# Performance work log

Hardware: AMD Instinct MI355X
Metric: run time of the kernel (lower is better)

## Reference

```python
import jax, jax.numpy as jnp
import numpy as np

SIGNAL_DIM = 64   # D
STATE_DIM = 64    # N
SEQ_LEN = 16384   # L
BATCH = 16


def _init_dplr_hippo(state_dim):
    """NumPy port of init_DPLR_HiPPO(signal_dim=1, state_dim). Returns Lambda,(N,) P,(N,) B,(N,1) complex64."""
    n = np.arange(state_dim, dtype=np.float64)
    A = np.zeros((state_dim, state_dim))
    for k in range(state_dim):
        A[k:, k] = np.sqrt(2.0 * np.arange(k, state_dim) + 1.0) * np.sqrt(2.0 * k + 1.0)
        A[k, k] = k + 1
    A = -A
    P = np.sqrt(n + 0.5)
    SI = A + P[:, None] * P[None, :]
    diag = np.diagonal(SI).copy()
    S = SI - np.diag(diag)
    eigvals, V = np.linalg.eigh(S * -1j)   # S*-1j is Hermitian
    Lam = diag + 1j * eigvals
    Vc = V.conj().T
    Pc = Vc @ P.astype(np.complex128)
    B = np.sqrt(2.0 * n + 1.0)[:, None]    # (N, 1): signal_dim=1, tied across channels
    Bc = Vc @ B.astype(np.complex128)
    return Lam.astype(np.complex64), Pc.astype(np.complex64), Bc.astype(np.complex64)


def _ri(x):
    # complex -> (..., 2) float32, matching torch.view_as_real parameter storage
    return jnp.stack([jnp.real(x), jnp.imag(x)], axis=-1).astype(jnp.float32)


def _to_c(x):
    return jax.lax.complex(x[..., 0], x[..., 1])


def setup_inputs() -> dict:
    key = jax.random.key(0)
    ku, kc1, kc2, kd, ks = jax.random.split(key, 5)
    Lam, P, B = _init_dplr_hippo(STATE_DIM)
    C = (jax.random.normal(kc1, (SIGNAL_DIM, STATE_DIM)) +
         1j * jax.random.normal(kc2, (SIGNAL_DIM, STATE_DIM))).astype(jnp.complex64)
    return {
        "u": jax.random.normal(ku, (BATCH, SEQ_LEN, SIGNAL_DIM), dtype=jnp.float32),
        "Lambda_ri": _ri(jnp.asarray(Lam)),      # (N, 2)
        "P_ri": _ri(jnp.asarray(P)),             # (N, 2)
        "B_ri": _ri(jnp.asarray(B)),             # (N, 1, 2)
        "C_ri": _ri(C),                          # (D, N, 2)
        "D_param": jax.random.normal(kd, (SIGNAL_DIM,), dtype=jnp.float32),
        "log_step": jnp.log(jax.random.uniform(ks, (1,), minval=0.001, maxval=0.1)).astype(jnp.float32),
    }


def reference(u, Lambda_ri, P_ri, B_ri, C_ri, D_param, log_step):
    Lam = _to_c(Lambda_ri)   # (N,)
    P = _to_c(P_ri)          # (N,)
    B = _to_c(B_ri)          # (N, 1)
    C = _to_c(C_ri)          # (D, N)
    L = u.shape[-2]

    step = jnp.exp(log_step)                                  # (1,)
    Omega = jnp.exp(-2j * jnp.pi * (jnp.arange(L) / L))       # (L,) roots of unity
    g = (2.0 / step) * ((1.0 - Omega) / (1.0 + Omega))        # (L,)

    # Batched Cauchy kernel: k_ab[l] = sum_n a_n * b_n / (g_l - Lambda_n)
    cauchy = 1.0 / (g[:, None] - Lam[None, :])                # (L, N)
    a0 = jnp.conj(C)        # (D, N)
    a1 = jnp.conj(P)        # (N,)
    b0 = B[:, 0]            # (N,)  == B.T row (signal_dim=1)
    b1 = P                  # (N,)
    k00 = jnp.einsum('dn,n,ln->dl', a0, b0, cauchy)
    k01 = jnp.einsum('dn,n,ln->dl', a0, b1, cauchy)
    k10 = jnp.einsum('n,n,ln->l', a1, b0, cauchy)
    k11 = jnp.einsum('n,n,ln->l', a1, b1, cauchy)

    evaluated = (2.0 / (1.0 + Omega)) * (k00 - k01 * (1.0 / (1.0 + k11)) * k10)  # (D, L)
    K = jnp.fft.ifft(evaluated, axis=-1).T.real               # (L, D) conv kernel

    # FFT convolution along time axis (zero-pad to 2L, linear convolution)
    ud = jnp.fft.rfft(jnp.pad(u, ((0, 0), (0, L), (0, 0))), axis=-2)
    Kd = jnp.fft.rfft(jnp.pad(K, ((0, L), (0, 0))), axis=-2)
    y = jnp.fft.irfft(ud * Kd, n=2 * L, axis=-2)[..., :L, :]
    return y + D_param * u
```

## Files before the change

kernel.cpp:

```cpp
#include <hip/hip_runtime.h>
#include <math.h>

#define MF 16384
#define HALF 8192

__device__ __forceinline__ float2 cmul(float2 a, float2 b){ return make_float2(a.x*b.x - a.y*b.y, a.x*b.y + a.y*b.x); }
__device__ __forceinline__ float2 cmulc(float2 a, float2 b){ return make_float2(a.x*b.x + a.y*b.y, a.y*b.x - a.x*b.y); }
__device__ __forceinline__ int rho4(int v){ return ((v & 3) << 2) | (v >> 2); }
__device__ __forceinline__ int sob(int k){
    return (rho4(k & 15) << 10) | (rho4((k >> 4) & 15) << 6) | (rho4((k >> 8) & 15) << 2) | (k >> 12);
}
__device__ __forceinline__ int ph(int e){ return e ^ ((e >> 4) & 3) ^ (((e >> 6) & 3) << 2); }

__device__ __forceinline__ void bf4f(float2&a,float2&b,float2&c,float2&d){
    float t0x=a.x+c.x, t0y=a.y+c.y, t2x=a.x-c.x, t2y=a.y-c.y;
    float t1x=b.x+d.x, t1y=b.y+d.y, t3x=b.x-d.x, t3y=b.y-d.y;
    a=make_float2(t0x+t1x,t0y+t1y);
    b=make_float2(t2x+t3y,t2y-t3x);
    c=make_float2(t0x-t1x,t0y-t1y);
    d=make_float2(t2x-t3y,t2y+t3x);
}
__device__ __forceinline__ void bf4i(float2&a,float2&b,float2&c,float2&d){
    float t0x=a.x+c.x, t0y=a.y+c.y, t2x=a.x-c.x, t2y=a.y-c.y;
    float t1x=b.x+d.x, t1y=b.y+d.y, t3x=b.x-d.x, t3y=b.y-d.y;
    a=make_float2(t0x+t1x,t0y+t1y);
    b=make_float2(t2x-t3y,t2y+t3x);
    c=make_float2(t0x-t1x,t0y-t1y);
    d=make_float2(t2x+t3y,t2y-t3x);
}

#define W16_1 make_float2(0.92387953251128674f, -0.38268343236508978f)
#define W16_2 make_float2(0.70710678118654752f, -0.70710678118654752f)
#define W16_3 make_float2(0.38268343236508978f, -0.92387953251128674f)
#define W16_6 make_float2(-0.70710678118654752f, -0.70710678118654752f)
#define W16_9 make_float2(-0.92387953251128674f, 0.38268343236508978f)

__device__ __forceinline__ void dft16_fwd(float2* x){
    bf4f(x[0],x[4],x[8],x[12]);
    bf4f(x[1],x[5],x[9],x[13]);
    bf4f(x[2],x[6],x[10],x[14]);
    bf4f(x[3],x[7],x[11],x[15]);
    x[5]=cmul(x[5],W16_1);  x[9]=cmul(x[9],W16_2);   x[13]=cmul(x[13],W16_3);
    x[6]=cmul(x[6],W16_2);  { float2 t=x[10]; x[10]=make_float2(t.y,-t.x); } x[14]=cmul(x[14],W16_6);
    x[7]=cmul(x[7],W16_3);  x[11]=cmul(x[11],W16_6); x[15]=cmul(x[15],W16_9);
    bf4f(x[0],x[1],x[2],x[3]);
    bf4f(x[4],x[5],x[6],x[7]);
    bf4f(x[8],x[9],x[10],x[11]);
    bf4f(x[12],x[13],x[14],x[15]);
}
__device__ __forceinline__ void dft16_inv(float2* x){
    bf4i(x[0],x[1],x[2],x[3]);
    bf4i(x[4],x[5],x[6],x[7]);
    bf4i(x[8],x[9],x[10],x[11]);
    bf4i(x[12],x[13],x[14],x[15]);
    x[5]=cmulc(x[5],W16_1); x[9]=cmulc(x[9],W16_2);  x[13]=cmulc(x[13],W16_3);
    x[6]=cmulc(x[6],W16_2); { float2 t=x[10]; x[10]=make_float2(-t.y,t.x); } x[14]=cmulc(x[14],W16_6);
    x[7]=cmulc(x[7],W16_3); x[11]=cmulc(x[11],W16_6); x[15]=cmulc(x[15],W16_9);
    bf4i(x[0],x[4],x[8],x[12]);
    bf4i(x[1],x[5],x[9],x[13]);
    bf4i(x[2],x[6],x[10],x[14]);
    bf4i(x[3],x[7],x[11],x[15]);
}

template<bool INV>
__device__ __forceinline__ void tw0_apply(float2* x, float2 w1){
    float2 w2=cmul(w1,w1), w4=cmul(w2,w2), w8=cmul(w4,w4);
    float2 w3=cmul(w2,w1), w5=cmul(w4,w1), w6=cmul(w4,w2), w7=cmul(w4,w3);
    float2 w9=cmul(w8,w1), w10=cmul(w8,w2), w11=cmul(w8,w3), w12=cmul(w8,w4);
    float2 w13=cmul(w8,w5), w14=cmul(w8,w6), w15=cmul(w8,w7);
    if (!INV){
        x[1]=cmul(x[1],w4);   x[2]=cmul(x[2],w8);   x[3]=cmul(x[3],w12);
        x[4]=cmul(x[4],w1);   x[5]=cmul(x[5],w5);   x[6]=cmul(x[6],w9);
        x[7]=cmul(x[7],w13);  x[8]=cmul(x[8],w2);   x[9]=cmul(x[9],w6);
        x[10]=cmul(x[10],w10);x[11]=cmul(x[11],w14);x[12]=cmul(x[12],w3);
        x[13]=cmul(x[13],w7); x[14]=cmul(x[14],w11);x[15]=cmul(x[15],w15);
    } else {
        x[1]=cmulc(x[1],w4);   x[2]=cmulc(x[2],w8);   x[3]=cmulc(x[3],w12);
        x[4]=cmulc(x[4],w1);   x[5]=cmulc(x[5],w5);   x[6]=cmulc(x[6],w9);
        x[7]=cmulc(x[7],w13);  x[8]=cmulc(x[8],w2);   x[9]=cmulc(x[9],w6);
        x[10]=cmulc(x[10],w10);x[11]=cmulc(x[11],w14);x[12]=cmulc(x[12],w3);
        x[13]=cmulc(x[13],w7); x[14]=cmulc(x[14],w11);x[15]=cmulc(x[15],w15);
    }
}

template<bool INV>
__device__ __forceinline__ void pass0(float2* A, float2 w1g, int tid){
    float2 x[16];
    int base = ph(tid);
    #pragma unroll
    for(int m=0;m<16;++m) x[m] = A[base + (m<<10)];
    if(!INV){ dft16_fwd(x); tw0_apply<false>(x, w1g); }
    else { tw0_apply<true>(x, w1g); dft16_inv(x); }
    #pragma unroll
    for(int m=0;m<16;++m) A[base + (m<<10)] = x[m];
}

template<bool INV>
__device__ __forceinline__ void pass1(float2* A, const float2* tw1s, int tid){
    float2 x[16];
    int i1 = tid & 63;
    int B = (tid >> 6) << 10;
    int i1x = i1 ^ ((i1 >> 4) & 3);
    int b0 = B | i1x;
    int b1 = B | 64 | (i1x ^ 4);
    int b2 = B | 128 | (i1x ^ 8);
    int b3 = B | 192 | (i1x ^ 12);
    x[0]=A[b0];     x[1]=A[b1];     x[2]=A[b2];     x[3]=A[b3];
    x[4]=A[b0+256]; x[5]=A[b1+256]; x[6]=A[b2+256]; x[7]=A[b3+256];
    x[8]=A[b0+512]; x[9]=A[b1+512]; x[10]=A[b2+512];x[11]=A[b3+512];
    x[12]=A[b0+768];x[13]=A[b1+768];x[14]=A[b2+768];x[15]=A[b3+768];
    if(!INV){
        dft16_fwd(x);
        #pragma unroll
        for(int j=1;j<16;++j) x[j] = cmul(x[j], tw1s[(j<<6)+i1]);
    } else {
        #pragma unroll
        for(int j=1;j<16;++j) x[j] = cmulc(x[j], tw1s[(j<<6)+i1]);
        dft16_inv(x);
    }
    A[b0]=x[0];     A[b1]=x[1];     A[b2]=x[2];     A[b3]=x[3];
    A[b0+256]=x[4]; A[b1+256]=x[5]; A[b2+256]=x[6]; A[b3+256]=x[7];
    A[b0+512]=x[8]; A[b1+512]=x[9]; A[b2+512]=x[10];A[b3+512]=x[11];
    A[b0+768]=x[12];A[b1+768]=x[13];A[b2+768]=x[14];A[b3+768]=x[15];
}

template<bool INV>
__device__ __forceinline__ void pass2(float2* A, const float2* tw2s, int tid){
    float2 x[16];
    int q = tid >> 2, j2 = tid & 3;
    int qb = q << 6, qa = q & 3;
    int c0 = qb | (j2 ^ 0);
    int c1 = qb | 16 | (j2 ^ 1);
    int c2 = qb | 32 | (j2 ^ 2);
    int c3 = qb | 48 | (j2 ^ 3);
    int r0 = (qa ^ 0) << 2, r1 = (qa ^ 1) << 2, r2 = (qa ^ 2) << 2, r3 = (qa ^ 3) << 2;
    x[0]=A[c0+r0];  x[1]=A[c0+r1];  x[2]=A[c0+r2];  x[3]=A[c0+r3];
    x[4]=A[c1+r0];  x[5]=A[c1+r1];  x[6]=A[c1+r2];  x[7]=A[c1+r3];
    x[8]=A[c2+r0];  x[9]=A[c2+r1];  x[10]=A[c2+r2]; x[11]=A[c2+r3];
    x[12]=A[c3+r0]; x[13]=A[c3+r1]; x[14]=A[c3+r2]; x[15]=A[c3+r3];
    if(!INV){
        dft16_fwd(x);
        #pragma unroll
        for(int j=1;j<16;++j) x[j] = cmul(x[j], tw2s[(j<<2)+j2]);
    } else {
        #pragma unroll
        for(int j=1;j<16;++j) x[j] = cmulc(x[j], tw2s[(j<<2)+j2]);
        dft16_inv(x);
    }
    A[c0+r0]=x[0];  A[c0+r1]=x[1];  A[c0+r2]=x[2];  A[c0+r3]=x[3];
    A[c1+r0]=x[4];  A[c1+r1]=x[5];  A[c1+r2]=x[6];  A[c1+r3]=x[7];
    A[c2+r0]=x[8];  A[c2+r1]=x[9];  A[c2+r2]=x[10]; A[c2+r3]=x[11];
    A[c3+r0]=x[12]; A[c3+r1]=x[13]; A[c3+r2]=x[14]; A[c3+r3]=x[15];
}

template<bool INV>
__device__ __forceinline__ void pass3(float2* A, int tid){
    int sgm = ((tid>>2)&3) ^ (((tid>>4)&3)<<2);
    #pragma unroll
    for(int rr=0; rr<4; ++rr){
        int base = (tid<<2) | (rr<<12);
        float2 a=A[(base|0)^sgm], b=A[(base|1)^sgm], c=A[(base|2)^sgm], d=A[(base|3)^sgm];
        if(!INV) bf4f(a,b,c,d); else bf4i(a,b,c,d);
        A[(base|0)^sgm]=a; A[(base|1)^sgm]=b; A[(base|2)^sgm]=c; A[(base|3)^sgm]=d;
    }
}

__global__ __launch_bounds__(1024) void k_evalinit(const float2* __restrict__ Lam, const float2* __restrict__ P,
        const float2* __restrict__ Bc, const float2* __restrict__ C,
        const float* __restrict__ log_step, float2* __restrict__ E,
        float2* __restrict__ baseg, float2* __restrict__ tw1g, float2* __restrict__ tw2g) {
    __shared__ float2 bTs[16][64];
    __shared__ float2 pTs[16][64];
    __shared__ float2 S10s[16], S11s[16];
    __shared__ float2 C_l[64][65];
    __shared__ float2 tile[16][65];
    int tid = threadIdx.x;
    if (blockIdx.x >= 256){
        const double TP = 6.2831853071795864769;
        double a = -TP * (double)tid / 16384.0;
        baseg[tid] = make_float2((float)cos(a), (float)sin(a));
        double a1 = -TP * (double)((tid & 63) * rho4(tid >> 6)) / 1024.0;
        tw1g[tid] = make_float2((float)cos(a1), (float)sin(a1));
        if (tid < 64){
            double a2 = -TP * (double)((tid & 3) * rho4(tid >> 2)) / 64.0;
            tw2g[tid] = make_float2((float)cos(a2), (float)sin(a2));
        }
        return;
    }
    int l0 = blockIdx.x * 64;
    float step = expf(log_step[0]);
    {
        int dq = tid >> 6, n = tid & 63;
        #pragma unroll
        for (int p = 0; p < 4; ++p) { int dd = dq + p * 16; C_l[n][dd] = C[dd * 64 + n]; }
    }
    __syncthreads();
    int w = tid >> 6;
    int lane = tid & 63;
    for (int p = 0; p < 4; ++p) {
        int l = l0 + p * 16 + w;
        float lf = (float)l * (1.0f / 16384.0f);
        float s2 = sinpif(lf), c2 = cospif(lf);
        float2 q1 = make_float2(2.0f*c2*c2, -2.0f*s2*c2);
        {
            int n = lane;
            float2 q2 = make_float2(4.0f*s2*s2, 4.0f*s2*c2);
            float2 ln = Lam[n];
            float2 lq = cmul(ln, q1);
            float2 den = make_float2(q2.x - step*lq.x, q2.y - step*lq.y);
            float idn = step / (den.x*den.x + den.y*den.y);
            float2 T = make_float2(den.x*idn, -den.y*idn);
            float2 bn = Bc[n], pn = P[n];
            float2 bT = cmul(bn, T), pT = cmul(pn, T);
            bTs[w][n] = bT; pTs[w][n] = pT;
            float2 s10 = make_float2(pn.x*bT.x + pn.y*bT.y, pn.x*bT.y - pn.y*bT.x);
            float2 s11 = make_float2(pn.x*pT.x + pn.y*pT.y, pn.x*pT.y - pn.y*pT.x);
            #pragma unroll
            for (int off = 32; off > 0; off >>= 1) {
                s10.x += __shfl_xor(s10.x, off);
                s10.y += __shfl_xor(s10.y, off);
                s11.x += __shfl_xor(s11.x, off);
                s11.y += __shfl_xor(s11.y, off);
            }
            if (n == 0) { S10s[w] = s10; S11s[w] = s11; }
        }
        __syncthreads();
        {
            int d = lane;
            float2 S00 = make_float2(0.f, 0.f), S01 = make_float2(0.f, 0.f);
            #pragma unroll 8
            for (int n = 0; n < 64; ++n) {
                float2 cn = C_l[n][d];
                float2 bT = bTs[w][n];
                float2 pT = pTs[w][n];
                S00.x += cn.x*bT.x + cn.y*bT.y;  S00.y += cn.x*bT.y - cn.y*bT.x;
                S01.x += cn.x*pT.x + cn.y*pT.y;  S01.y += cn.x*pT.y - cn.y*pT.x;
            }
            float2 S10 = S10s[w], S11 = S11s[w];
            float2 k11 = cmul(q1, S11); k11.x += 1.0f;
            float2 k10q = cmul(q1, S10);
            float ik = 1.0f / (k11.x*k11.x + k11.y*k11.y);
            float2 quo = make_float2((k10q.x*k11.x + k10q.y*k11.y) * ik,
                                     (k10q.y*k11.x - k10q.x*k11.y) * ik);
            float2 corr = cmul(S01, quo);
            tile[w][d] = make_float2(2.0f*(S00.x - corr.x), 2.0f*(S00.y - corr.y));
        }
        __syncthreads();
        {
            int lo = tid & 15, dq = tid >> 4;
            E[(size_t)dq * MF + l0 + p * 16 + lo] = tile[lo][dq];
        }
        __syncthreads();
    }
}

union MidShm {
    struct { float2 A[MF]; float2 tw1s[1024]; float2 tw2s[64]; } p;
    float t[256][65];
};

__global__ __launch_bounds__(1024) void k_mid(const float2* __restrict__ E, float4* __restrict__ Ktab,
        const float2* __restrict__ baseg, const float2* __restrict__ tw1g, const float2* __restrict__ tw2g,
        const float* __restrict__ u, float* __restrict__ uT) {
    __shared__ MidShm sh;
    int tid = threadIdx.x;
    if (blockIdx.x >= 64){
        int cid = blockIdx.x - 64;
        int b = cid >> 6, t0c = (cid & 63) << 8;
        const float* ub = u + ((size_t)(b * MF + t0c)) * 64;
        #pragma unroll
        for (int it = 0; it < 16; ++it){
            int tl = it * 16 + (tid >> 6), dl = tid & 63;
            sh.t[tl][dl] = ub[(size_t)tl * 64 + dl];
        }
        __syncthreads();
        float* dst = uT + (size_t)b * 64 * MF + t0c;
        #pragma unroll
        for (int it = 0; it < 16; ++it){
            int dd = (tid >> 8) + it * 4, tl = tid & 255;
            dst[(size_t)dd * MF + tl] = sh.t[tl][dd];
        }
        return;
    }
    float2* A = sh.p.A;
    float2* tw1s = sh.p.tw1s;
    float2* tw2s = sh.p.tw2s;
    float2 w1g = baseg[tid];
    tw1s[tid] = tw1g[tid];
    if (tid < 64) tw2s[tid] = tw2g[tid];
    int d = blockIdx.x;
    const float2* Ed = E + (size_t)d * MF;
    #pragma unroll
    for (int r = 0; r < 16; ++r) { int l = tid + (r << 10); A[ph(sob(l))] = Ed[l]; }
    __syncthreads();
    pass3<true>(A, tid); __syncthreads();
    pass2<true>(A, tw2s, tid); __syncthreads();
    pass1<true>(A, tw1s, tid); __syncthreads();
    pass0<true>(A, w1g, tid); __syncthreads();
    const float s = 1.0f / (float)MF;
    float2 rv[8];
    #pragma unroll
    for (int r = 0; r < 8; ++r) {
        int t = tid + (r << 10);
        rv[r] = make_float2(A[ph(2*t)].x * s, A[ph(2*t+1)].x * s);
    }
    __syncthreads();
    int pht = ph(tid);
    #pragma unroll
    for (int r = 0; r < 16; ++r) A[pht + (r << 10)] = (r < 8) ? rv[r] : make_float2(0.f, 0.f);
    __syncthreads();
    pass0<false>(A, w1g, tid); __syncthreads();
    pass1<false>(A, tw1s, tid); __syncthreads();
    pass2<false>(A, tw2s, tid); __syncthreads();
    pass3<false>(A, tid); __syncthreads();
    float4* Kd = Ktab + (size_t)d * MF;
    int Cbits = (rho4(tid >> 6) << 4) | (rho4((tid >> 2) & 15) << 8) | ((tid & 3) << 12);
    const float ksc = 1.0f / (float)MF;
    #pragma unroll
    for (int r = 0; r < 16; ++r) {
        int k = Cbits | rho4(r);
        int kp = (MF - k) & (MF - 1);
        int p = sob(kp);
        float kf = (float)k * (1.0f / 16384.0f);
        float2 w = make_float2(cospif(kf), -sinpif(kf));
        float2 Zk = A[pht + (r << 10)];
        float2 Zm = A[ph(p)]; Zm.y = -Zm.y;
        float2 Ue = make_float2(0.5f*(Zk.x + Zm.x), 0.5f*(Zk.y + Zm.y));
        float2 dd = make_float2(Zk.x - Zm.x, Zk.y - Zm.y);
        float2 Uo = make_float2(0.5f*dd.y, -0.5f*dd.x);
        float2 t2 = cmul(w, Uo);
        Kd[tid + (r << 10)] = make_float4((Ue.x + t2.x)*ksc, (Ue.y + t2.y)*ksc,
                                          (Ue.x - t2.x)*ksc, (Ue.y - t2.y)*ksc);
    }
}

template<bool TRANS>
__global__ __launch_bounds__(1024) void k_conv(const float* __restrict__ u, const float* __restrict__ uT,
        const float4* __restrict__ Ktab, const float* __restrict__ Dp,
        float* __restrict__ yT, float* __restrict__ yout,
        const float2* __restrict__ baseg, const float2* __restrict__ tw1g, const float2* __restrict__ tw2g) {
    __shared__ float2 A[MF];
    __shared__ float2 tw1s[1024];
    __shared__ float2 tw2s[64];
    int tid = threadIdx.x;
    float2 w1g = baseg[tid];
    tw1s[tid] = tw1g[tid];
    if (tid < 64) tw2s[tid] = tw2g[tid];
    int bid = blockIdx.x;
    int vb = ((bid & 7) << 7) | (bid >> 3);
    int d = vb >> 4, b = vb & 15;
    int bd = (b << 6) | d;
    int base = ph(tid);
    const float2* src = (const float2*)(uT + (size_t)bd * MF);
    const float* ub = u + ((size_t)b * MF) * 64 + d;
    {
        float2 x[16];
        #pragma unroll
        for (int m = 0; m < 16; ++m){
            if (m < 8){
                if (TRANS) x[m] = src[tid + (m << 10)];
                else { int t = tid + (m << 10); x[m] = make_float2(ub[(size_t)(2*t)*64], ub[(size_t)(2*t+1)*64]); }
            } else x[m] = make_float2(0.f, 0.f);
        }
        dft16_fwd(x);
        tw0_apply<false>(x, w1g);
        #pragma unroll
        for (int m = 0; m < 16; ++m) A[base + (m << 10)] = x[m];
    }
    __syncthreads();
    pass1<false>(A, tw1s, tid); __syncthreads();
    pass2<false>(A, tw2s, tid); __syncthreads();
    const float4* Kd = Ktab + (size_t)d * MF;
    float4 kd[16];
    #pragma unroll
    for (int r = 0; r < 16; ++r) kd[r] = Kd[tid + (r << 10)];
    pass3<false>(A, tid); __syncthreads();
    int Cbits = (rho4(tid >> 6) << 4) | (rho4((tid >> 2) & 15) << 8) | ((tid & 3) << 12);
    float2 Wr[16];
    #pragma unroll
    for (int r = 0; r < 16; ++r) {
        int k = Cbits | rho4(r);
        int kp = (MF - k) & (MF - 1);
        int p = sob(kp);
        float kf = (float)k * (1.0f / 16384.0f);
        float2 w = make_float2(cospif(kf), -sinpif(kf));
        float2 Zk = A[base + (r << 10)];
        float2 Zm = A[ph(p)]; Zm.y = -Zm.y;
        float2 Ue = make_float2(0.5f*(Zk.x + Zm.x), 0.5f*(Zk.y + Zm.y));
        float2 dd = make_float2(Zk.x - Zm.x, Zk.y - Zm.y);
        float2 Uo = make_float2(0.5f*dd.y, -0.5f*dd.x);
        float2 t2 = cmul(w, Uo);
        float2 X0 = make_float2(Ue.x + t2.x, Ue.y + t2.y);
        float2 X1 = make_float2(Ue.x - t2.x, Ue.y - t2.y);
        float2 Y0 = cmul(X0, make_float2(kd[r].x, kd[r].y));
        float2 Y1 = cmul(X1, make_float2(kd[r].z, kd[r].w));
        float2 Ey = make_float2(0.5f*(Y0.x + Y1.x), 0.5f*(Y0.y + Y1.y));
        float2 Dy = make_float2(Y0.x - Y1.x, Y0.y - Y1.y);
        float2 Oy = cmulc(Dy, w);
        Oy.x *= 0.5f; Oy.y *= 0.5f;
        Wr[r] = make_float2(Ey.x - Oy.y, Ey.y + Oy.x);
    }
    __syncthreads();
    #pragma unroll
    for (int r = 0; r < 16; ++r) A[base + (r << 10)] = Wr[r];
    __syncthreads();
    pass3<true>(A, tid); __syncthreads();
    pass2<true>(A, tw2s, tid); __syncthreads();
    pass1<true>(A, tw1s, tid); __syncthreads();
    {
        float2 x[16];
        #pragma unroll
        for (int m = 0; m < 16; ++m) x[m] = A[base + (m << 10)];
        tw0_apply<true>(x, w1g);
        dft16_inv(x);
        float Dd = Dp[d];
        if (TRANS){
            float2* dst = (float2*)(yT + (size_t)bd * MF);
            #pragma unroll
            for (int m = 0; m < 8; ++m){
                float2 s2 = src[tid + (m << 10)];
                dst[tid + (m << 10)] = make_float2(x[m].x + Dd * s2.x, x[m].y + Dd * s2.y);
            }
        } else {
            float* yb = yout + ((size_t)b * MF) * 64 + d;
            #pragma unroll
            for (int m = 0; m < 8; ++m){
                int t = tid + (m << 10);
                yb[(size_t)(2*t)*64]   = x[m].x + Dd * ub[(size_t)(2*t)*64];
                yb[(size_t)(2*t+1)*64] = x[m].y + Dd * ub[(size_t)(2*t+1)*64];
            }
        }
    }
}

__global__ void k_out(const float* __restrict__ yT, float* __restrict__ y) {
    __shared__ float tile[64][65];
    int b = blockIdx.y, t0 = blockIdx.x * 64, tid = threadIdx.x;
    #pragma unroll
    for (int k2 = 0; k2 < 16; ++k2) {
        int idx = tid + k2 * 256;
        int dl = idx >> 6, tl = idx & 63;
        tile[dl][tl] = yT[((size_t)b * 64 + dl) * MF + t0 + tl];
    }
    __syncthreads();
    #pragma unroll
    for (int k2 = 0; k2 < 16; ++k2) {
        int idx = tid + k2 * 256;
        int tl = idx >> 6, dl = idx & 63;
        y[((size_t)(b * MF + t0 + tl)) * 64 + dl] = tile[dl][tl];
    }
}

extern "C" void kernel_launch(void* const* d_in, const int* in_sizes, int n_in,
                              void* d_out, int out_size, void* d_ws, size_t ws_size,
                              hipStream_t stream) {
    const float*  u   = (const float*)d_in[0];
    const float2* Lam = (const float2*)d_in[1];
    const float2* P   = (const float2*)d_in[2];
    const float2* Bc  = (const float2*)d_in[3];
    const float2* C   = (const float2*)d_in[4];
    const float*  Dp  = (const float*)d_in[5];
    const float*  ls  = (const float*)d_in[6];
    float* y = (float*)d_out;
    char* ws = (char*)d_ws;

    size_t off = 0;
    float2* baseg = (float2*)(ws + off); off += (size_t)1024 * sizeof(float2);
    float2* tw1g  = (float2*)(ws + off); off += (size_t)1024 * sizeof(float2);
    float2* tw2g  = (float2*)(ws + off); off += (size_t)64 * sizeof(float2) + 512;
    float2* E     = (float2*)(ws + off); off += (size_t)64 * MF * sizeof(float2);
    float4* Ktab  = (float4*)(ws + off); off += (size_t)64 * MF * sizeof(float4);
    float*  uT    = (float*) (ws + off); off += (size_t)1024 * MF * sizeof(float);
    float*  yT    = (float*) (ws + off); off += (size_t)1024 * MF * sizeof(float);
    bool trans = (ws_size >= off);

    k_evalinit<<<257, 1024, 0, stream>>>(Lam, P, Bc, C, ls, E, baseg, tw1g, tw2g);
    k_mid<<<trans ? 1088 : 64, 1024, 0, stream>>>(E, Ktab, baseg, tw1g, tw2g, u, uT);

    if (trans) {
        k_conv<true><<<1024, 1024, 0, stream>>>(u, uT, Ktab, Dp, yT, y, baseg, tw1g, tw2g);
        k_out<<<dim3(MF / 64, 16), 256, 0, stream>>>(yT, y);
    } else {
        k_conv<false><<<1024, 1024, 0, stream>>>(u, nullptr, Ktab, Dp, nullptr, y, baseg, tw1g, tw2g);
    }
}
```

Before: 299.8 us.

## Fuse last FFT pass into pointwise multiply and compute twiddles by recurrence

In the convolution kernel, the final radix-4 forward pass and the first inverse pass are folded into the pointwise spectrum-multiply stage. This removes two shared-memory round trips and their barriers. Pass1 and pass2 twiddles are now derived from a single base twiddle per thread, which shrinks the shared twiddle tables, while k_mid keeps the old table-driven passes. The D*u skip term moves from k_conv into the k_out transpose kernel, which now reads u again from global memory in exchange for skipping the uT read in k_conv.

```diff
diff --git a/kernel.cpp b/kernel.cpp
--- a/kernel.cpp
+++ b/kernel.cpp
@@ -96,7 +96,7 @@
 }
 
 template<bool INV>
-__device__ __forceinline__ void pass1(float2* A, const float2* tw1s, int tid){
+__device__ __forceinline__ void pass1(float2* A, const float2* basP1, int tid){
     float2 x[16];
     int i1 = tid & 63;
     int B = (tid >> 6) << 10;
@@ -109,15 +109,9 @@
     x[4]=A[b0+256]; x[5]=A[b1+256]; x[6]=A[b2+256]; x[7]=A[b3+256];
     x[8]=A[b0+512]; x[9]=A[b1+512]; x[10]=A[b2+512];x[11]=A[b3+512];
     x[12]=A[b0+768];x[13]=A[b1+768];x[14]=A[b2+768];x[15]=A[b3+768];
-    if(!INV){
-        dft16_fwd(x);
-        #pragma unroll
-        for(int j=1;j<16;++j) x[j] = cmul(x[j], tw1s[(j<<6)+i1]);
-    } else {
-        #pragma unroll
-        for(int j=1;j<16;++j) x[j] = cmulc(x[j], tw1s[(j<<6)+i1]);
-        dft16_inv(x);
-    }
+    float2 w1 = basP1[i1];
+    if(!INV){ dft16_fwd(x); tw0_apply<false>(x, w1); }
+    else { tw0_apply<true>(x, w1); dft16_inv(x); }
     A[b0]=x[0];     A[b1]=x[1];     A[b2]=x[2];     A[b3]=x[3];
     A[b0+256]=x[4]; A[b1+256]=x[5]; A[b2+256]=x[6]; A[b3+256]=x[7];
     A[b0+512]=x[8]; A[b1+512]=x[9]; A[b2+512]=x[10];A[b3+512]=x[11];
@@ -125,7 +119,7 @@
 }
 
 template<bool INV>
-__device__ __forceinline__ void pass2(float2* A, const float2* tw2s, int tid){
+__device__ __forceinline__ void pass2(float2* A, const float2* basP2, int tid){
     float2 x[16];
     int q = tid >> 2, j2 = tid & 3;
     int qb = q << 6, qa = q & 3;
@@ -138,15 +132,9 @@
     x[4]=A[c1+r0];  x[5]=A[c1+r1];  x[6]=A[c1+r2];  x[7]=A[c1+r3];
     x[8]=A[c2+r0];  x[9]=A[c2+r1];  x[10]=A[c2+r2]; x[11]=A[c2+r3];
     x[12]=A[c3+r0]; x[13]=A[c3+r1]; x[14]=A[c3+r2]; x[15]=A[c3+r3];
-    if(!INV){
-        dft16_fwd(x);
-        #pragma unroll
-        for(int j=1;j<16;++j) x[j] = cmul(x[j], tw2s[(j<<2)+j2]);
-    } else {
-        #pragma unroll
-        for(int j=1;j<16;++j) x[j] = cmulc(x[j], tw2s[(j<<2)+j2]);
-        dft16_inv(x);
-    }
+    float2 w1 = basP2[j2];
+    if(!INV){ dft16_fwd(x); tw0_apply<false>(x, w1); }
+    else { tw0_apply<true>(x, w1); dft16_inv(x); }
     A[c0+r0]=x[0];  A[c0+r1]=x[1];  A[c0+r2]=x[2];  A[c0+r3]=x[3];
     A[c1+r0]=x[4];  A[c1+r1]=x[5];  A[c1+r2]=x[6];  A[c1+r3]=x[7];
     A[c2+r0]=x[8];  A[c2+r1]=x[9];  A[c2+r2]=x[10]; A[c2+r3]=x[11];
@@ -163,6 +151,35 @@
         if(!INV) bf4f(a,b,c,d); else bf4i(a,b,c,d);
         A[(base|0)^sgm]=a; A[(base|1)^sgm]=b; A[(base|2)^sgm]=c; A[(base|3)^sgm]=d;
     }
+}
+
+__device__ __forceinline__ float2 pw_slot(float2 Zk, float2 Zm, float4 kd, float2 w){
+    Zm.y = -Zm.y;
+    float2 Ue = make_float2(0.5f*(Zk.x+Zm.x), 0.5f*(Zk.y+Zm.y));
+    float2 dd = make_float2(Zk.x-Zm.x, Zk.y-Zm.y);
+    float2 Uo = make_float2(0.5f*dd.y, -0.5f*dd.x);
+    float2 t2 = cmul(w, Uo);
+    float2 X0 = make_float2(Ue.x+t2.x, Ue.y+t2.y);
+    float2 X1 = make_float2(Ue.x-t2.x, Ue.y-t2.y);
+    float2 Y0 = cmul(X0, make_float2(kd.x,kd.y));
+    float2 Y1 = cmul(X1, make_float2(kd.z,kd.w));
+    float2 Ey = make_float2(0.5f*(Y0.x+Y1.x), 0.5f*(Y0.y+Y1.y));
+    float2 Dy = make_float2(Y0.x-Y1.x, Y0.y-Y1.y);
+    float2 Oy = cmulc(Dy, w);
+    return make_float2(Ey.x - 0.5f*Oy.y, Ey.y + 0.5f*Oy.x);
+}
+template<int I>
+__device__ __forceinline__ float2 wslot(float2 wb){
+    const float r2 = 0.70710678118654752f;
+    if (I==0) return wb;
+    if (I==1) return make_float2((wb.x+wb.y)*r2, (wb.y-wb.x)*r2);
+    if (I==2) return make_float2(wb.y, -wb.x);
+    return make_float2((wb.y-wb.x)*r2, -(wb.x+wb.y)*r2);
+}
+__device__ __forceinline__ float2 sel4(int i, float2 a, float2 b, float2 c, float2 d){
+    float2 ab = (i & 1) ? b : a;
+    float2 cd = (i & 1) ? d : c;
+    return (i & 2) ? cd : ab;
 }
 
 __global__ __launch_bounds__(1024) void k_evalinit(const float2* __restrict__ Lam, const float2* __restrict__ P,
@@ -259,6 +276,57 @@
     float t[256][65];
 };
 
+template<bool INV>
+__device__ __forceinline__ void pass1t(float2* A, const float2* tw1s, int tid){
+    float2 x[16];
+    int i1 = tid & 63;
+    int B = (tid >> 6) << 10;
+    int i1x = i1 ^ ((i1 >> 4) & 3);
+    int b0 = B | i1x, b1 = B | 64 | (i1x ^ 4), b2 = B | 128 | (i1x ^ 8), b3 = B | 192 | (i1x ^ 12);
+    x[0]=A[b0];     x[1]=A[b1];     x[2]=A[b2];     x[3]=A[b3];
+    x[4]=A[b0+256]; x[5]=A[b1+256]; x[6]=A[b2+256]; x[7]=A[b3+256];
+    x[8]=A[b0+512]; x[9]=A[b1+512]; x[10]=A[b2+512];x[11]=A[b3+512];
+    x[12]=A[b0+768];x[13]=A[b1+768];x[14]=A[b2+768];x[15]=A[b3+768];
+    if(!INV){
+        dft16_fwd(x);
+        #pragma unroll
+        for(int j=1;j<16;++j) x[j] = cmul(x[j], tw1s[(j<<6)+i1]);
+    } else {
+        #pragma unroll
+        for(int j=1;j<16;++j) x[j] = cmulc(x[j], tw1s[(j<<6)+i1]);
+        dft16_inv(x);
+    }
+    A[b0]=x[0];     A[b1]=x[1];     A[b2]=x[2];     A[b3]=x[3];
+    A[b0+256]=x[4]; A[b1+256]=x[5]; A[b2+256]=x[6]; A[b3+256]=x[7];
+    A[b0+512]=x[8]; A[b1+512]=x[9]; A[b2+512]=x[10];A[b3+512]=x[11];
+    A[b0+768]=x[12];A[b1+768]=x[13];A[b2+768]=x[14];A[b3+768]=x[15];
+}
+template<bool INV>
+__device__ __forceinline__ void pass2t(float2* A, const float2* tw2s, int tid){
+    float2 x[16];
+    int q = tid >> 2, j2 = tid & 3;
+    int qb = q << 6, qa = q & 3;
+    int c0 = qb | (j2 ^ 0), c1 = qb | 16 | (j2 ^ 1), c2 = qb | 32 | (j2 ^ 2), c3 = qb | 48 | (j2 ^ 3);
+    int r0 = (qa ^ 0) << 2, r1 = (qa ^ 1) << 2, r2 = (qa ^ 2) << 2, r3 = (qa ^ 3) << 2;
+    x[0]=A[c0+r0];  x[1]=A[c0+r1];  x[2]=A[c0+r2];  x[3]=A[c0+r3];
+    x[4]=A[c1+r0];  x[5]=A[c1+r1];  x[6]=A[c1+r2];  x[7]=A[c1+r3];
+    x[8]=A[c2+r0];  x[9]=A[c2+r1];  x[10]=A[c2+r2]; x[11]=A[c2+r3];
+    x[12]=A[c3+r0]; x[13]=A[c3+r1]; x[14]=A[c3+r2]; x[15]=A[c3+r3];
+    if(!INV){
+        dft16_fwd(x);
+        #pragma unroll
+        for(int j=1;j<16;++j) x[j] = cmul(x[j], tw2s[(j<<2)+j2]);
+    } else {
+        #pragma unroll
+        for(int j=1;j<16;++j) x[j] = cmulc(x[j], tw2s[(j<<2)+j2]);
+        dft16_inv(x);
+    }
+    A[c0+r0]=x[0];  A[c0+r1]=x[1];  A[c0+r2]=x[2];  A[c0+r3]=x[3];
+    A[c1+r0]=x[4];  A[c1+r1]=x[5];  A[c1+r2]=x[6];  A[c1+r3]=x[7];
+    A[c2+r0]=x[8];  A[c2+r1]=x[9];  A[c2+r2]=x[10]; A[c2+r3]=x[11];
+    A[c3+r0]=x[12]; A[c3+r1]=x[13]; A[c3+r2]=x[14]; A[c3+r3]=x[15];
+}
+
 __global__ __launch_bounds__(1024) void k_mid(const float2* __restrict__ E, float4* __restrict__ Ktab,
         const float2* __restrict__ baseg, const float2* __restrict__ tw1g, const float2* __restrict__ tw2g,
         const float* __restrict__ u, float* __restrict__ uT) {
@@ -294,8 +362,8 @@
     for (int r = 0; r < 16; ++r) { int l = tid + (r << 10); A[ph(sob(l))] = Ed[l]; }
     __syncthreads();
     pass3<true>(A, tid); __syncthreads();
-    pass2<true>(A, tw2s, tid); __syncthreads();
-    pass1<true>(A, tw1s, tid); __syncthreads();
+    pass2t<true>(A, tw2s, tid); __syncthreads();
+    pass1t<true>(A, tw1s, tid); __syncthreads();
     pass0<true>(A, w1g, tid); __syncthreads();
     const float s = 1.0f / (float)MF;
     float2 rv[8];
@@ -310,8 +378,8 @@
     for (int r = 0; r < 16; ++r) A[pht + (r << 10)] = (r < 8) ? rv[r] : make_float2(0.f, 0.f);
     __syncthreads();
     pass0<false>(A, w1g, tid); __syncthreads();
-    pass1<false>(A, tw1s, tid); __syncthreads();
-    pass2<false>(A, tw2s, tid); __syncthreads();
+    pass1t<false>(A, tw1s, tid); __syncthreads();
+    pass2t<false>(A, tw2s, tid); __syncthreads();
     pass3<false>(A, tid); __syncthreads();
     float4* Kd = Ktab + (size_t)d * MF;
     int Cbits = (rho4(tid >> 6) << 4) | (rho4((tid >> 2) & 15) << 8) | ((tid & 3) << 12);
@@ -337,15 +405,14 @@
 template<bool TRANS>
 __global__ __launch_bounds__(1024) void k_conv(const float* __restrict__ u, const float* __restrict__ uT,
         const float4* __restrict__ Ktab, const float* __restrict__ Dp,
-        float* __restrict__ yT, float* __restrict__ yout,
-        const float2* __restrict__ baseg, const float2* __restrict__ tw1g, const float2* __restrict__ tw2g) {
+        float* __restrict__ yT, float* __restrict__ yout, const float2* __restrict__ baseg) {
     __shared__ float2 A[MF];
-    __shared__ float2 tw1s[1024];
-    __shared__ float2 tw2s[64];
+    __shared__ float2 basP1[64];
+    __shared__ float2 basP2[4];
     int tid = threadIdx.x;
     float2 w1g = baseg[tid];
-    tw1s[tid] = tw1g[tid];
-    if (tid < 64) tw2s[tid] = tw2g[tid];
+    if (tid < 64) basP1[tid] = baseg[tid << 4];
+    if (tid < 4)  basP2[tid] = baseg[tid << 8];
     int bid = blockIdx.x;
     int vb = ((bid & 7) << 7) | (bid >> 3);
     int d = vb >> 4, b = vb & 15;
@@ -368,60 +435,61 @@
         for (int m = 0; m < 16; ++m) A[base + (m << 10)] = x[m];
     }
     __syncthreads();
-    pass1<false>(A, tw1s, tid); __syncthreads();
-    pass2<false>(A, tw2s, tid); __syncthreads();
-    const float4* Kd = Ktab + (size_t)d * MF;
-    float4 kd[16];
-    #pragma unroll
-    for (int r = 0; r < 16; ++r) kd[r] = Kd[tid + (r << 10)];
-    pass3<false>(A, tid); __syncthreads();
-    int Cbits = (rho4(tid >> 6) << 4) | (rho4((tid >> 2) & 15) << 8) | ((tid & 3) << 12);
-    float2 Wr[16];
-    #pragma unroll
-    for (int r = 0; r < 16; ++r) {
-        int k = Cbits | rho4(r);
-        int kp = (MF - k) & (MF - 1);
-        int p = sob(kp);
-        float kf = (float)k * (1.0f / 16384.0f);
-        float2 w = make_float2(cospif(kf), -sinpif(kf));
-        float2 Zk = A[base + (r << 10)];
-        float2 Zm = A[ph(p)]; Zm.y = -Zm.y;
-        float2 Ue = make_float2(0.5f*(Zk.x + Zm.x), 0.5f*(Zk.y + Zm.y));
-        float2 dd = make_float2(Zk.x - Zm.x, Zk.y - Zm.y);
-        float2 Uo = make_float2(0.5f*dd.y, -0.5f*dd.x);
-        float2 t2 = cmul(w, Uo);
-        float2 X0 = make_float2(Ue.x + t2.x, Ue.y + t2.y);
-        float2 X1 = make_float2(Ue.x - t2.x, Ue.y - t2.y);
-        float2 Y0 = cmul(X0, make_float2(kd[r].x, kd[r].y));
-        float2 Y1 = cmul(X1, make_float2(kd[r].z, kd[r].w));
-        float2 Ey = make_float2(0.5f*(Y0.x + Y1.x), 0.5f*(Y0.y + Y1.y));
-        float2 Dy = make_float2(Y0.x - Y1.x, Y0.y - Y1.y);
-        float2 Oy = cmulc(Dy, w);
-        Oy.x *= 0.5f; Oy.y *= 0.5f;
-        Wr[r] = make_float2(Ey.x - Oy.y, Ey.y + Oy.x);
-    }
-    __syncthreads();
-    #pragma unroll
-    for (int r = 0; r < 16; ++r) A[base + (r << 10)] = Wr[r];
-    __syncthreads();
-    pass3<true>(A, tid); __syncthreads();
-    pass2<true>(A, tw2s, tid); __syncthreads();
-    pass1<true>(A, tw1s, tid); __syncthreads();
+    pass1<false>(A, basP1, tid); __syncthreads();
+    pass2<false>(A, basP2, tid); __syncthreads();
+    {
+        const float4* Kdp = Ktab + (size_t)d * MF;
+        float2 res[16];
+        #pragma unroll
+        for (int q = 0; q < 4; ++q){
+            int uq = tid + (q << 10);
+            int s0 = uq << 2;
+            float2 za = A[ph(s0)],   zb = A[ph(s0+1)], zc = A[ph(s0+2)], zd = A[ph(s0+3)];
+            bf4f(za, zb, zc, zd);
+            int k0 = rho4(uq >> 8) | (rho4((uq >> 4) & 15) << 4) | (rho4(uq & 15) << 8);
+            int p0 = sob((MF - k0) & (MF - 1));
+            int pb = p0 & ~3, jp0 = p0 & 3;
+            float2 pa = A[ph(pb)], pbv = A[ph(pb+1)], pc = A[ph(pb+2)], pd = A[ph(pb+3)];
+            bf4f(pa, pbv, pc, pd);
+            float kbf = (float)k0 * (1.0f / 16384.0f);
+            float2 wb = make_float2(cospif(kbf), -sinpif(kbf));
+            float4 kd0 = Kdp[s0], kd1 = Kdp[s0+1], kd2 = Kdp[s0+2], kd3 = Kdp[s0+3];
+            float2 zp0 = sel4(jp0,           pa, pbv, pc, pd);
+            float2 zp1 = sel4((jp0 + 3) & 3, pa, pbv, pc, pd);
+            float2 zp2 = sel4((jp0 + 2) & 3, pa, pbv, pc, pd);
+            float2 zp3 = sel4((jp0 + 1) & 3, pa, pbv, pc, pd);
+            float2 rr0 = pw_slot(za, zp0, kd0, wslot<0>(wb));
+            float2 rr1 = pw_slot(zb, zp1, kd1, wslot<1>(wb));
+            float2 rr2 = pw_slot(zc, zp2, kd2, wslot<2>(wb));
+            float2 rr3 = pw_slot(zd, zp3, kd3, wslot<3>(wb));
+            bf4i(rr0, rr1, rr2, rr3);
+            res[q*4+0]=rr0; res[q*4+1]=rr1; res[q*4+2]=rr2; res[q*4+3]=rr3;
+        }
+        __syncthreads();
+        #pragma unroll
+        for (int q = 0; q < 4; ++q){
+            int s0 = (tid + (q << 10)) << 2;
+            A[ph(s0)]   = res[q*4+0];
+            A[ph(s0+1)] = res[q*4+1];
+            A[ph(s0+2)] = res[q*4+2];
+            A[ph(s0+3)] = res[q*4+3];
+        }
+    }
+    __syncthreads();
+    pass2<true>(A, basP2, tid); __syncthreads();
+    pass1<true>(A, basP1, tid); __syncthreads();
     {
         float2 x[16];
         #pragma unroll
         for (int m = 0; m < 16; ++m) x[m] = A[base + (m << 10)];
         tw0_apply<true>(x, w1g);
         dft16_inv(x);
-        float Dd = Dp[d];
         if (TRANS){
             float2* dst = (float2*)(yT + (size_t)bd * MF);
             #pragma unroll
-            for (int m = 0; m < 8; ++m){
-                float2 s2 = src[tid + (m << 10)];
-                dst[tid + (m << 10)] = make_float2(x[m].x + Dd * s2.x, x[m].y + Dd * s2.y);
-            }
+            for (int m = 0; m < 8; ++m) dst[tid + (m << 10)] = x[m];
         } else {
+            float Dd = Dp[d];
             float* yb = yout + ((size_t)b * MF) * 64 + d;
             #pragma unroll
             for (int m = 0; m < 8; ++m){
@@ -433,7 +501,8 @@
     }
 }
 
-__global__ void k_out(const float* __restrict__ yT, float* __restrict__ y) {
+__global__ void k_out(const float* __restrict__ yT, const float* __restrict__ u,
+                      const float* __restrict__ Dp, float* __restrict__ y) {
     __shared__ float tile[64][65];
     int b = blockIdx.y, t0 = blockIdx.x * 64, tid = threadIdx.x;
     #pragma unroll
@@ -447,7 +516,8 @@
     for (int k2 = 0; k2 < 16; ++k2) {
         int idx = tid + k2 * 256;
         int tl = idx >> 6, dl = idx & 63;
-        y[((size_t)(b * MF + t0 + tl)) * 64 + dl] = tile[dl][tl];
+        size_t gi = ((size_t)(b * MF + t0 + tl)) * 64 + dl;
+        y[gi] = tile[dl][tl] + Dp[dl] * u[gi];
     }
 }
 
@@ -478,9 +548,9 @@
     k_mid<<<trans ? 1088 : 64, 1024, 0, stream>>>(E, Ktab, baseg, tw1g, tw2g, u, uT);
 
     if (trans) {
-        k_conv<true><<<1024, 1024, 0, stream>>>(u, uT, Ktab, Dp, yT, y, baseg, tw1g, tw2g);
-        k_out<<<dim3(MF / 64, 16), 256, 0, stream>>>(yT, y);
+        k_conv<true><<<1024, 1024, 0, stream>>>(u, uT, Ktab, Dp, yT, y, baseg);
+        k_out<<<dim3(MF / 64, 16), 256, 0, stream>>>(yT, u, Dp, y);
     } else {
-        k_conv<false><<<1024, 1024, 0, stream>>>(u, nullptr, Ktab, Dp, nullptr, y, baseg, tw1g, tw2g);
-    }
-}
+        k_conv<false><<<1024, 1024, 0, stream>>>(u, nullptr, Ktab, Dp, nullptr, y, baseg);
+    }
+}
```

Measured after the change: 325.5 us. 1.09x slower.
